# Optimization experiments

Hardware: AMD Instinct MI355X
Metric: run time of the kernel (lower is better)

## Reference

```python
import jax, jax.numpy as jnp
import numpy as np

NUM_EXPERTS = 8
EXPERTS_PER_TOK = 2

def setup_inputs() -> dict:
    key = jax.random.key(0)
    k1, k2, k3, k4, k5 = jax.random.split(key, 5)
    B, T, D, F, E = 4, 1024, 2048, 1024, NUM_EXPERTS
    return {
        "x": jax.random.normal(k1, (B, T, D), dtype=jnp.float32),
        "router_w": jax.random.normal(k2, (D, E), dtype=jnp.float32) * 0.02,
        "gate_proj": jax.random.normal(k3, (E, D, F), dtype=jnp.float32) * 0.02,
        "up_proj": jax.random.normal(k4, (E, D, F), dtype=jnp.float32) * 0.02,
        "down_proj": jax.random.normal(k5, (E, F, D), dtype=jnp.float32) * 0.02,
    }

def reference(x, router_w, gate_proj, up_proj, down_proj):
    E, K = NUM_EXPERTS, EXPERTS_PER_TOK
    # Router: softmax over experts, take top-k, renormalize.
    scores = jnp.einsum('btd,de->bte', x, router_w).astype(jnp.float32)
    routing_weights, routing_idx = jax.lax.top_k(jax.nn.softmax(scores, axis=-1), K)
    routing_weights = (routing_weights / jnp.sum(routing_weights, axis=-1, keepdims=True)).astype(x.dtype)
    # one_hot: [B,T,K,E]. Sum over K gives 0/1 dispatch mask [B,T,E]
    # (top-k indices are distinct). Weighted sum gives combine weights.
    onehot = jax.nn.one_hot(routing_idx, E, dtype=x.dtype)
    dispatch_mask = jnp.sum(onehot, axis=2)                      # [B,T,E]
    combine_weights = jnp.einsum('btke,btk->bte', onehot, routing_weights)
    # Dense masked dispatch (same math as original einsum with size-1 I axis).
    dispatched = x[:, :, None, :] * dispatch_mask[..., None]     # [B,T,E,D]
    # SwiGLU FFN for every expert, batched over E.
    gate = jnp.einsum('bted,edf->btef', dispatched, gate_proj)
    up = jnp.einsum('bted,edf->btef', dispatched, up_proj)
    act = jax.nn.silu(gate) * up                                 # [B,T,E,F]
    expert_out = jnp.einsum('btef,efd->bted', act, down_proj)    # [B,T,E,D]
    # Combine: weights already include the dispatch mask via one-hot.
    return jnp.einsum('bted,bte->btd', expert_out, combine_weights)
```

## Files before the change

kernel.cpp:

```cpp
#include <hip/hip_runtime.h>
#include <stdint.h>

#define BT 4096
#define DMODEL 2048
#define FDIM 1024
#define NEXP 8
#define NA (BT * 2)
#define MAXTILES 72

typedef __attribute__((ext_vector_type(8))) __bf16 bf16x8;
typedef __attribute__((ext_vector_type(4))) float f32x4;

__device__ __forceinline__ unsigned short f2bf(float f) {
  union { float f; unsigned int u; } v; v.f = f;
  unsigned int u = v.u;
  unsigned int r = (u + 0x7fffu + ((u >> 16) & 1u)) >> 16;
  return (unsigned short)r;
}
__device__ __forceinline__ float bf2f(unsigned short h) {
  union { unsigned int u; float f; } v; v.u = ((unsigned int)h) << 16;
  return v.f;
}

__device__ __forceinline__ void g2l16(const void* g, void* l) {
  __builtin_amdgcn_global_load_lds((const __attribute__((address_space(1))) void*)g,
                                   (__attribute__((address_space(3))) void*)l, 16, 0, 0);
}


__global__ void k_router(const float* __restrict__ x, const float* __restrict__ rw,
                         unsigned short* __restrict__ xbf,
                         int* __restrict__ tok_e, float* __restrict__ tok_w) {
  int wid = threadIdx.x >> 6;
  int lane = threadIdx.x & 63;
  int t = blockIdx.x * 4 + wid;
  float acc[8];
#pragma unroll
  for (int e = 0; e < 8; e++) acc[e] = 0.0f;
  const float* xr = x + (size_t)t * DMODEL;
  unsigned short* xbr = xbf + (size_t)t * DMODEL;
#pragma unroll
  for (int d0 = lane * 4; d0 < DMODEL; d0 += 256) {
    float4 xv = *(const float4*)(xr + d0);
    ushort4 o = make_ushort4(f2bf(xv.x), f2bf(xv.y), f2bf(xv.z), f2bf(xv.w));
    *(ushort4*)(xbr + d0) = o;
    const float* xs = &xv.x;
#pragma unroll
    for (int j = 0; j < 4; j++) {
      const float4* r4 = (const float4*)(rw + (size_t)(d0 + j) * NEXP);
      float4 ra = r4[0], rb = r4[1];
      float xj = xs[j];
      acc[0] += xj * ra.x; acc[1] += xj * ra.y; acc[2] += xj * ra.z; acc[3] += xj * ra.w;
      acc[4] += xj * rb.x; acc[5] += xj * rb.y; acc[6] += xj * rb.z; acc[7] += xj * rb.w;
    }
  }
#pragma unroll
  for (int e = 0; e < 8; e++) {
    float v = acc[e];
#pragma unroll
    for (int off = 32; off > 0; off >>= 1) v += __shfl_xor(v, off);
    acc[e] = v;
  }
  if (lane == 0) {
    int e0 = 0; float s0 = acc[0];
#pragma unroll
    for (int e = 1; e < 8; e++) if (acc[e] > s0) { s0 = acc[e]; e0 = e; }
    int e1 = (e0 == 0) ? 1 : 0; float s1 = acc[e1];
#pragma unroll
    for (int e = 0; e < 8; e++) if (e != e0 && acc[e] > s1) { s1 = acc[e]; e1 = e; }
    float w0 = 1.0f / (1.0f + __expf(s1 - s0));
    tok_e[t * 2] = e0; tok_e[t * 2 + 1] = e1;
    tok_w[t * 2] = w0; tok_w[t * 2 + 1] = 1.0f - w0;
  }
}

__global__ void k_scanbuild(const int* __restrict__ tok_e, int* __restrict__ offsets,
                            int* __restrict__ tile_e, int* __restrict__ tile_y,
                            int* __restrict__ ntiles, int* __restrict__ cursors) {
  __shared__ int hist[NEXP];
  int tid = threadIdx.x;
  if (tid < NEXP) hist[tid] = 0;
  __syncthreads();
  for (int i = tid; i < NA; i += 256) atomicAdd(&hist[tok_e[i]], 1);
  __syncthreads();
  if (tid == 0) {
    int s = 0;
    for (int e = 0; e < NEXP; e++) { offsets[e] = s; s += hist[e]; }
    offsets[NEXP] = s;
    int idx = 0;
    for (int e = 0; e < NEXP; e++) {
      int nt = (hist[e] + 127) >> 7;
      for (int y = 0; y < nt; y++) { tile_e[idx] = e; tile_y[idx] = y; idx++; }
    }
    *ntiles = idx;
    for (int i = idx; i < MAXTILES; i++) { tile_e[i] = 0; tile_y[i] = 0; }
  }
  if (tid < NEXP) cursors[tid] = 0;
}

__global__ void k_scatter(const int* __restrict__ tok_e, const float* __restrict__ tok_w,
                          const int* __restrict__ offsets, int* __restrict__ cursors,
                          int* __restrict__ assign_token, float* __restrict__ assign_w,
                          int* __restrict__ tok2pos) {
  int i = blockIdx.x * 256 + threadIdx.x;
  if (i >= NA) return;
  int e = tok_e[i];
  int pos = offsets[e] + atomicAdd(&cursors[e], 1);
  assign_token[pos] = i >> 1;
  assign_w[pos] = tok_w[i];
  tok2pos[i] = pos;
}

__global__ void k_transpose_all(const float* __restrict__ gw, const float* __restrict__ uw,
                                const float* __restrict__ dw,
                                unsigned short* __restrict__ wtgu,
                                unsigned short* __restrict__ wtd) {
  __shared__ float tile[64][65];
  int z = blockIdx.y;
  const float* src; unsigned short* dst; int N, K, Kd;
  if (z < 8)       { src = gw + (size_t)z * DMODEL * FDIM;        dst = wtgu + (size_t)z * 2 * FDIM * DMODEL;        N = FDIM;   K = DMODEL; Kd = DMODEL; }
  else if (z < 16) { src = uw + (size_t)(z - 8) * DMODEL * FDIM;  dst = wtgu + (size_t)(z - 8) * 2 * FDIM * DMODEL;  N = FDIM;   K = DMODEL; Kd = DMODEL; }
  else             { src = dw + (size_t)(z - 16) * FDIM * DMODEL; dst = wtd + (size_t)(z - 16) * FDIM * DMODEL;      N = DMODEL; K = FDIM;   Kd = FDIM; }
  int ntx = N >> 6;
  int bx = blockIdx.x;
  int n0 = (bx % ntx) * 64, k0 = (bx / ntx) * 64;
  int rr = threadIdx.x >> 4, cc = threadIdx.x & 15;
#pragma unroll
  for (int i = 0; i < 4; i++) {
    int k = rr + i * 16;
    float4 v = *(const float4*)(src + (size_t)(k0 + k) * N + n0 + cc * 4);
    tile[k][cc * 4 + 0] = v.x; tile[k][cc * 4 + 1] = v.y;
    tile[k][cc * 4 + 2] = v.z; tile[k][cc * 4 + 3] = v.w;
  }
  __syncthreads();
#pragma unroll
  for (int i = 0; i < 4; i++) {
    int n = rr + i * 16;
    int gr = n0 + n;
    int orow;
    if (z < 8)       orow = ((gr & ~31) << 1) + (gr & 31);
    else if (z < 16) orow = ((gr & ~31) << 1) + 32 + (gr & 31);
    else             orow = gr;
    ushort4 o = make_ushort4(f2bf(tile[cc * 4 + 0][n]), f2bf(tile[cc * 4 + 1][n]),
                             f2bf(tile[cc * 4 + 2][n]), f2bf(tile[cc * 4 + 3][n]));
    *(ushort4*)(dst + (size_t)orow * Kd + k0 + cc * 4) = o;
  }
}


__global__ __launch_bounds__(256, 4) void k_gemm1(
    const unsigned short* __restrict__ xbf,
    const unsigned short* __restrict__ wtgu,
    const int* __restrict__ offsets,
    const int* __restrict__ tile_e, const int* __restrict__ tile_y,
    const int* __restrict__ ntiles,
    const int* __restrict__ assign_token,
    unsigned short* __restrict__ act) {
  const int ti = blockIdx.y;
  if (ti >= *ntiles) return;
  const int e = tile_e[ti];
  const int row_beg = offsets[e], row_end = offsets[e + 1];
  const int m_base = row_beg + tile_y[ti] * 128;
  const int n_base = blockIdx.x * 128;

  __shared__ unsigned short As[128][64];
  __shared__ unsigned short Bs[128][64];

  const int tid = threadIdx.x;
  const int lane = tid & 63, wid = tid >> 6;
  const int wr = wid >> 1, wc = wid & 1;
  const int srow = wid * 8 + (lane >> 3);
  const int scol_d = (lane & 7) * 8;
  const int scol_s = ((lane & 7) ^ (lane >> 3)) * 8;
  const int sw = (lane & 7) * 8;

  const unsigned short* wb = wtgu + (size_t)e * 2 * FDIM * DMODEL + (size_t)n_base * DMODEL;

  size_t arow[4];
#pragma unroll
  for (int i = 0; i < 4; i++) {
    int slot = m_base + i * 32 + srow;
    if (slot >= row_end) slot = row_end - 1;
    arow[i] = (size_t)assign_token[slot] * DMODEL;
  }

  f32x4 acc[4][4];
#pragma unroll
  for (int m = 0; m < 4; m++)
#pragma unroll
    for (int n = 0; n < 4; n++) acc[m][n] = f32x4{0.f, 0.f, 0.f, 0.f};

  for (int k0 = 0; k0 < DMODEL; k0 += 64) {
    __syncthreads();
#pragma unroll
    for (int i = 0; i < 4; i++)
      g2l16(xbf + arow[i] + k0 + scol_s, &As[i * 32 + srow][scol_d]);
#pragma unroll
    for (int i = 0; i < 4; i++)
      g2l16(wb + (size_t)(i * 32 + srow) * DMODEL + k0 + scol_s, &Bs[i * 32 + srow][scol_d]);
    __syncthreads();

#pragma unroll
    for (int kk = 0; kk < 2; kk++) {
      const int ko = kk * 32 + (lane >> 4) * 8;
      bf16x8 a[4], b[4];
#pragma unroll
      for (int m = 0; m < 4; m++)
        a[m] = *(const bf16x8*)&As[wr * 64 + m * 16 + (lane & 15)][ko ^ sw];
#pragma unroll
      for (int n = 0; n < 4; n++)
        b[n] = *(const bf16x8*)&Bs[wc * 64 + n * 16 + (lane & 15)][ko ^ sw];
#pragma unroll
      for (int m = 0; m < 4; m++)
#pragma unroll
        for (int n = 0; n < 4; n++)
          acc[m][n] = __builtin_amdgcn_mfma_f32_16x16x32_bf16(a[m], b[n], acc[m][n], 0, 0, 0);
    }
  }

  const int cr = (lane >> 4) * 4;
  const int ccc = lane & 15;
#pragma unroll
  for (int m = 0; m < 4; m++) {
#pragma unroll
    for (int j = 0; j < 4; j++) {
      int slot = m_base + wr * 64 + m * 16 + cr + j;
      if (slot < row_end) {
        unsigned short* dst = act + (size_t)slot * FDIM + (n_base >> 1) + wc * 32 + ccc;
#pragma unroll
        for (int n = 0; n < 2; n++) {
          float g = acc[m][n][j], u = acc[m][n + 2][j];
          float h = (g / (1.0f + __expf(-g))) * u;
          dst[n * 16] = f2bf(h);
        }
      }
    }
  }
}


__global__ __launch_bounds__(256, 4) void k_gemm2(
    const unsigned short* __restrict__ act,
    const unsigned short* __restrict__ wtd,
    const int* __restrict__ offsets,
    const int* __restrict__ tile_e, const int* __restrict__ tile_y,
    const int* __restrict__ ntiles,
    const float* __restrict__ assign_w,
    unsigned short* __restrict__ out_pa) {
  const int ti = blockIdx.y;
  if (ti >= *ntiles) return;
  const int e = tile_e[ti];
  const int row_beg = offsets[e], row_end = offsets[e + 1];
  const int m_base = row_beg + tile_y[ti] * 128;
  const int n_base = blockIdx.x * 128;

  __shared__ unsigned short As[128][64];
  __shared__ unsigned short Bs[128][64];

  const int tid = threadIdx.x;
  const int lane = tid & 63, wid = tid >> 6;
  const int wr = wid >> 1, wc = wid & 1;
  const int srow = wid * 8 + (lane >> 3);
  const int scol_d = (lane & 7) * 8;
  const int scol_s = ((lane & 7) ^ (lane >> 3)) * 8;
  const int sw = (lane & 7) * 8;

  const unsigned short* wd_e = wtd + (size_t)e * DMODEL * FDIM + (size_t)n_base * FDIM;

  size_t arow[4];
#pragma unroll
  for (int i = 0; i < 4; i++) {
    int slot = m_base + i * 32 + srow;
    if (slot >= row_end) slot = row_end - 1;
    arow[i] = (size_t)slot * FDIM;
  }

  f32x4 acc[4][4];
#pragma unroll
  for (int m = 0; m < 4; m++)
#pragma unroll
    for (int n = 0; n < 4; n++) acc[m][n] = f32x4{0.f, 0.f, 0.f, 0.f};

  for (int k0 = 0; k0 < FDIM; k0 += 64) {
    __syncthreads();
#pragma unroll
    for (int i = 0; i < 4; i++)
      g2l16(act + arow[i] + k0 + scol_s, &As[i * 32 + srow][scol_d]);
#pragma unroll
    for (int i = 0; i < 4; i++)
      g2l16(wd_e + (size_t)(i * 32 + srow) * FDIM + k0 + scol_s, &Bs[i * 32 + srow][scol_d]);
    __syncthreads();

#pragma unroll
    for (int kk = 0; kk < 2; kk++) {
      const int ko = kk * 32 + (lane >> 4) * 8;
      bf16x8 a[4], b[4];
#pragma unroll
      for (int m = 0; m < 4; m++)
        a[m] = *(const bf16x8*)&As[wr * 64 + m * 16 + (lane & 15)][ko ^ sw];
#pragma unroll
      for (int n = 0; n < 4; n++)
        b[n] = *(const bf16x8*)&Bs[wc * 64 + n * 16 + (lane & 15)][ko ^ sw];
#pragma unroll
      for (int m = 0; m < 4; m++)
#pragma unroll
        for (int n = 0; n < 4; n++)
          acc[m][n] = __builtin_amdgcn_mfma_f32_16x16x32_bf16(a[m], b[n], acc[m][n], 0, 0, 0);
    }
  }

  const int cr = (lane >> 4) * 4;
  const int ccc = lane & 15;
#pragma unroll
  for (int m = 0; m < 4; m++) {
#pragma unroll
    for (int j = 0; j < 4; j++) {
      int slot = m_base + wr * 64 + m * 16 + cr + j;
      if (slot < row_end) {
        float w = assign_w[slot];
        unsigned short* dst = out_pa + (size_t)slot * DMODEL + n_base + wc * 64 + ccc;
#pragma unroll
        for (int n = 0; n < 4; n++)
          dst[n * 16] = f2bf(acc[m][n][j] * w);
      }
    }
  }
}

__global__ void k_combine(const unsigned short* __restrict__ out_pa,
                          const int* __restrict__ tok2pos,
                          float* __restrict__ out) {
  int t = blockIdx.x;
  int p0 = tok2pos[t * 2], p1 = tok2pos[t * 2 + 1];
  int c = threadIdx.x;
  const ushort4* a = (const ushort4*)(out_pa + (size_t)p0 * DMODEL + c * 8);
  const ushort4* b = (const ushort4*)(out_pa + (size_t)p1 * DMODEL + c * 8);
  ushort4 a0 = a[0], a1 = a[1], b0 = b[0], b1 = b[1];
  float* o = out + (size_t)t * DMODEL + c * 8;
  o[0] = bf2f(a0.x) + bf2f(b0.x);
  o[1] = bf2f(a0.y) + bf2f(b0.y);
  o[2] = bf2f(a0.z) + bf2f(b0.z);
  o[3] = bf2f(a0.w) + bf2f(b0.w);
  o[4] = bf2f(a1.x) + bf2f(b1.x);
  o[5] = bf2f(a1.y) + bf2f(b1.y);
  o[6] = bf2f(a1.z) + bf2f(b1.z);
  o[7] = bf2f(a1.w) + bf2f(b1.w);
}


extern "C" void kernel_launch(void* const* d_in, const int* in_sizes, int n_in,
                              void* d_out, int out_size, void* d_ws, size_t ws_size,
                              hipStream_t stream) {
  const float* x  = (const float*)d_in[0];
  const float* rw = (const float*)d_in[1];
  const float* gw = (const float*)d_in[2];
  const float* uw = (const float*)d_in[3];
  const float* dw = (const float*)d_in[4];
  float* out = (float*)d_out;

  char* ws = (char*)d_ws;
  size_t off = 0;
  auto alloc = [&](size_t bytes) {
    size_t o = off;
    off += (bytes + 255) & ~(size_t)255;
    return o;
  };
  unsigned short* xbf    = (unsigned short*)(ws + alloc((size_t)BT * DMODEL * 2));
  unsigned short* wtgu   = (unsigned short*)(ws + alloc((size_t)NEXP * 2 * FDIM * DMODEL * 2));
  unsigned short* wtd    = (unsigned short*)(ws + alloc((size_t)NEXP * DMODEL * FDIM * 2));
  unsigned short* act    = (unsigned short*)(ws + alloc((size_t)NA * FDIM * 2));
  unsigned short* out_pa = (unsigned short*)(ws + alloc((size_t)NA * DMODEL * 2));
  int*   offsets = (int*)(ws + alloc((NEXP + 1) * 4));
  int*   cursors = (int*)(ws + alloc(NEXP * 4));
  int*   tok_e   = (int*)(ws + alloc(NA * 4));
  float* tok_w   = (float*)(ws + alloc(NA * 4));
  int*   assign_token = (int*)(ws + alloc(NA * 4));
  float* assign_w     = (float*)(ws + alloc(NA * 4));
  int*   tok2pos      = (int*)(ws + alloc(NA * 4));
  int*   tile_e       = (int*)(ws + alloc(MAXTILES * 4));
  int*   tile_y       = (int*)(ws + alloc(MAXTILES * 4));
  int*   ntiles       = (int*)(ws + alloc(4));
  if (off > ws_size) return;

  k_router<<<BT / 4, 256, 0, stream>>>(x, rw, xbf, tok_e, tok_w);
  k_scanbuild<<<1, 256, 0, stream>>>(tok_e, offsets, tile_e, tile_y, ntiles, cursors);
  k_scatter<<<NA / 256, 256, 0, stream>>>(tok_e, tok_w, offsets, cursors,
                                          assign_token, assign_w, tok2pos);
  k_transpose_all<<<dim3(512, 24), 256, 0, stream>>>(gw, uw, dw, wtgu, wtd);
  k_gemm1<<<dim3(DMODEL * 2 / 128 / 2, MAXTILES), 256, 0, stream>>>(xbf, wtgu, offsets,
                                                                    tile_e, tile_y, ntiles,
                                                                    assign_token, act);
  k_gemm2<<<dim3(DMODEL / 128, MAXTILES), 256, 0, stream>>>(act, wtd, offsets,
                                                            tile_e, tile_y, ntiles,
                                                            assign_w, out_pa);
  k_combine<<<BT, 256, 0, stream>>>(out_pa, tok2pos, out);
}
```

Before: 301.0 us.

## Double-buffer GEMM tiles and fuse combine into down-proj via atomic adds

Both expert GEMMs now double-buffer their LDS tiles, issuing the next tile's global-to-LDS loads before computing on the current one, and raise wave priority around the MFMA block. The separate combine kernel and its bf16 per-assignment intermediate are removed: gemm2 atomically adds its weighted fp32 results straight into a zeroed output. This drops one kernel launch and a large intermediate write and read, at the cost of float atomics, a memset, and lower occupancy from the doubled shared memory.

```diff
diff --git a/kernel.cpp b/kernel.cpp
--- a/kernel.cpp
+++ b/kernel.cpp
@@ -11,15 +11,15 @@
 typedef __attribute__((ext_vector_type(8))) __bf16 bf16x8;
 typedef __attribute__((ext_vector_type(4))) float f32x4;
 
+#define FENCE() asm volatile("" ::: "memory")
+#define BARRIER() do { FENCE(); __builtin_amdgcn_s_barrier(); FENCE(); } while (0)
+#define VMCNT0()  asm volatile("s_waitcnt vmcnt(0)" ::: "memory")
+
 __device__ __forceinline__ unsigned short f2bf(float f) {
   union { float f; unsigned int u; } v; v.f = f;
   unsigned int u = v.u;
   unsigned int r = (u + 0x7fffu + ((u >> 16) & 1u)) >> 16;
   return (unsigned short)r;
-}
-__device__ __forceinline__ float bf2f(unsigned short h) {
-  union { unsigned int u; float f; } v; v.u = ((unsigned int)h) << 16;
-  return v.f;
 }
 
 __device__ __forceinline__ void g2l16(const void* g, void* l) {
@@ -100,15 +100,13 @@
 
 __global__ void k_scatter(const int* __restrict__ tok_e, const float* __restrict__ tok_w,
                           const int* __restrict__ offsets, int* __restrict__ cursors,
-                          int* __restrict__ assign_token, float* __restrict__ assign_w,
-                          int* __restrict__ tok2pos) {
+                          int* __restrict__ assign_token, float* __restrict__ assign_w) {
   int i = blockIdx.x * 256 + threadIdx.x;
   if (i >= NA) return;
   int e = tok_e[i];
   int pos = offsets[e] + atomicAdd(&cursors[e], 1);
   assign_token[pos] = i >> 1;
   assign_w[pos] = tok_w[i];
-  tok2pos[i] = pos;
 }
 
 __global__ void k_transpose_all(const float* __restrict__ gw, const float* __restrict__ uw,
@@ -117,10 +115,10 @@
                                 unsigned short* __restrict__ wtd) {
   __shared__ float tile[64][65];
   int z = blockIdx.y;
-  const float* src; unsigned short* dst; int N, K, Kd;
-  if (z < 8)       { src = gw + (size_t)z * DMODEL * FDIM;        dst = wtgu + (size_t)z * 2 * FDIM * DMODEL;        N = FDIM;   K = DMODEL; Kd = DMODEL; }
-  else if (z < 16) { src = uw + (size_t)(z - 8) * DMODEL * FDIM;  dst = wtgu + (size_t)(z - 8) * 2 * FDIM * DMODEL;  N = FDIM;   K = DMODEL; Kd = DMODEL; }
-  else             { src = dw + (size_t)(z - 16) * FDIM * DMODEL; dst = wtd + (size_t)(z - 16) * FDIM * DMODEL;      N = DMODEL; K = FDIM;   Kd = FDIM; }
+  const float* src; unsigned short* dst; int N, Kd;
+  if (z < 8)       { src = gw + (size_t)z * DMODEL * FDIM;        dst = wtgu + (size_t)z * 2 * FDIM * DMODEL;        N = FDIM;   Kd = DMODEL; }
+  else if (z < 16) { src = uw + (size_t)(z - 8) * DMODEL * FDIM;  dst = wtgu + (size_t)(z - 8) * 2 * FDIM * DMODEL;  N = FDIM;   Kd = DMODEL; }
+  else             { src = dw + (size_t)(z - 16) * FDIM * DMODEL; dst = wtd + (size_t)(z - 16) * FDIM * DMODEL;      N = DMODEL; Kd = FDIM; }
   int ntx = N >> 6;
   int bx = blockIdx.x;
   int n0 = (bx % ntx) * 64, k0 = (bx / ntx) * 64;
@@ -148,7 +146,7 @@
 }
 
 
-__global__ __launch_bounds__(256, 4) void k_gemm1(
+__global__ __launch_bounds__(256, 2) void k_gemm1(
     const unsigned short* __restrict__ xbf,
     const unsigned short* __restrict__ wtgu,
     const int* __restrict__ offsets,
@@ -163,8 +161,8 @@
   const int m_base = row_beg + tile_y[ti] * 128;
   const int n_base = blockIdx.x * 128;
 
-  __shared__ unsigned short As[128][64];
-  __shared__ unsigned short Bs[128][64];
+  __shared__ unsigned short As[2][128][64];
+  __shared__ unsigned short Bs[2][128][64];
 
   const int tid = threadIdx.x;
   const int lane = tid & 63, wid = tid >> 6;
@@ -190,32 +188,41 @@
 #pragma unroll
     for (int n = 0; n < 4; n++) acc[m][n] = f32x4{0.f, 0.f, 0.f, 0.f};
 
-  for (int k0 = 0; k0 < DMODEL; k0 += 64) {
-    __syncthreads();
+  auto stage = [&](int buf, int k0) {
 #pragma unroll
     for (int i = 0; i < 4; i++)
-      g2l16(xbf + arow[i] + k0 + scol_s, &As[i * 32 + srow][scol_d]);
+      g2l16(xbf + arow[i] + k0 + scol_s, &As[buf][i * 32 + srow][scol_d]);
 #pragma unroll
     for (int i = 0; i < 4; i++)
-      g2l16(wb + (size_t)(i * 32 + srow) * DMODEL + k0 + scol_s, &Bs[i * 32 + srow][scol_d]);
-    __syncthreads();
-
+      g2l16(wb + (size_t)(i * 32 + srow) * DMODEL + k0 + scol_s, &Bs[buf][i * 32 + srow][scol_d]);
+  };
+
+  const int NT = DMODEL / 64;
+  stage(0, 0);
+  VMCNT0(); BARRIER();
+
+  for (int t = 0; t < NT; ++t) {
+    const int cur = t & 1, nxt = cur ^ 1;
+    if (t + 1 < NT) stage(nxt, (t + 1) * 64);
 #pragma unroll
     for (int kk = 0; kk < 2; kk++) {
       const int ko = kk * 32 + (lane >> 4) * 8;
       bf16x8 a[4], b[4];
 #pragma unroll
       for (int m = 0; m < 4; m++)
-        a[m] = *(const bf16x8*)&As[wr * 64 + m * 16 + (lane & 15)][ko ^ sw];
+        a[m] = *(const bf16x8*)&As[cur][wr * 64 + m * 16 + (lane & 15)][ko ^ sw];
 #pragma unroll
       for (int n = 0; n < 4; n++)
-        b[n] = *(const bf16x8*)&Bs[wc * 64 + n * 16 + (lane & 15)][ko ^ sw];
+        b[n] = *(const bf16x8*)&Bs[cur][wc * 64 + n * 16 + (lane & 15)][ko ^ sw];
+      __builtin_amdgcn_s_setprio(1);
 #pragma unroll
       for (int m = 0; m < 4; m++)
 #pragma unroll
         for (int n = 0; n < 4; n++)
           acc[m][n] = __builtin_amdgcn_mfma_f32_16x16x32_bf16(a[m], b[n], acc[m][n], 0, 0, 0);
-    }
+      __builtin_amdgcn_s_setprio(0);
+    }
+    VMCNT0(); BARRIER();
   }
 
   const int cr = (lane >> 4) * 4;
@@ -239,14 +246,15 @@
 }
 
 
-__global__ __launch_bounds__(256, 4) void k_gemm2(
+__global__ __launch_bounds__(256, 2) void k_gemm2(
     const unsigned short* __restrict__ act,
     const unsigned short* __restrict__ wtd,
     const int* __restrict__ offsets,
     const int* __restrict__ tile_e, const int* __restrict__ tile_y,
     const int* __restrict__ ntiles,
+    const int* __restrict__ assign_token,
     const float* __restrict__ assign_w,
-    unsigned short* __restrict__ out_pa) {
+    float* __restrict__ out) {
   const int ti = blockIdx.y;
   if (ti >= *ntiles) return;
   const int e = tile_e[ti];
@@ -254,8 +262,8 @@
   const int m_base = row_beg + tile_y[ti] * 128;
   const int n_base = blockIdx.x * 128;
 
-  __shared__ unsigned short As[128][64];
-  __shared__ unsigned short Bs[128][64];
+  __shared__ unsigned short As[2][128][64];
+  __shared__ unsigned short Bs[2][128][64];
 
   const int tid = threadIdx.x;
   const int lane = tid & 63, wid = tid >> 6;
@@ -281,32 +289,41 @@
 #pragma unroll
     for (int n = 0; n < 4; n++) acc[m][n] = f32x4{0.f, 0.f, 0.f, 0.f};
 
-  for (int k0 = 0; k0 < FDIM; k0 += 64) {
-    __syncthreads();
+  auto stage = [&](int buf, int k0) {
 #pragma unroll
     for (int i = 0; i < 4; i++)
-      g2l16(act + arow[i] + k0 + scol_s, &As[i * 32 + srow][scol_d]);
+      g2l16(act + arow[i] + k0 + scol_s, &As[buf][i * 32 + srow][scol_d]);
 #pragma unroll
     for (int i = 0; i < 4; i++)
-      g2l16(wd_e + (size_t)(i * 32 + srow) * FDIM + k0 + scol_s, &Bs[i * 32 + srow][scol_d]);
-    __syncthreads();
-
+      g2l16(wd_e + (size_t)(i * 32 + srow) * FDIM + k0 + scol_s, &Bs[buf][i * 32 + srow][scol_d]);
+  };
+
+  const int NT = FDIM / 64;
+  stage(0, 0);
+  VMCNT0(); BARRIER();
+
+  for (int t = 0; t < NT; ++t) {
+    const int cur = t & 1, nxt = cur ^ 1;
+    if (t + 1 < NT) stage(nxt, (t + 1) * 64);
 #pragma unroll
     for (int kk = 0; kk < 2; kk++) {
       const int ko = kk * 32 + (lane >> 4) * 8;
       bf16x8 a[4], b[4];
 #pragma unroll
       for (int m = 0; m < 4; m++)
-        a[m] = *(const bf16x8*)&As[wr * 64 + m * 16 + (lane & 15)][ko ^ sw];
+        a[m] = *(const bf16x8*)&As[cur][wr * 64 + m * 16 + (lane & 15)][ko ^ sw];
 #pragma unroll
       for (int n = 0; n < 4; n++)
-        b[n] = *(const bf16x8*)&Bs[wc * 64 + n * 16 + (lane & 15)][ko ^ sw];
+        b[n] = *(const bf16x8*)&Bs[cur][wc * 64 + n * 16 + (lane & 15)][ko ^ sw];
+      __builtin_amdgcn_s_setprio(1);
 #pragma unroll
       for (int m = 0; m < 4; m++)
 #pragma unroll
         for (int n = 0; n < 4; n++)
           acc[m][n] = __builtin_amdgcn_mfma_f32_16x16x32_bf16(a[m], b[n], acc[m][n], 0, 0, 0);
-    }
+      __builtin_amdgcn_s_setprio(0);
+    }
+    VMCNT0(); BARRIER();
   }
 
   const int cr = (lane >> 4) * 4;
@@ -317,34 +334,15 @@
     for (int j = 0; j < 4; j++) {
       int slot = m_base + wr * 64 + m * 16 + cr + j;
       if (slot < row_end) {
+        int tok = assign_token[slot];
         float w = assign_w[slot];
-        unsigned short* dst = out_pa + (size_t)slot * DMODEL + n_base + wc * 64 + ccc;
+        float* dst = out + (size_t)tok * DMODEL + n_base + wc * 64 + ccc;
 #pragma unroll
         for (int n = 0; n < 4; n++)
-          dst[n * 16] = f2bf(acc[m][n][j] * w);
+          atomicAdd(&dst[n * 16], acc[m][n][j] * w);
       }
     }
   }
-}
-
-__global__ void k_combine(const unsigned short* __restrict__ out_pa,
-                          const int* __restrict__ tok2pos,
-                          float* __restrict__ out) {
-  int t = blockIdx.x;
-  int p0 = tok2pos[t * 2], p1 = tok2pos[t * 2 + 1];
-  int c = threadIdx.x;
-  const ushort4* a = (const ushort4*)(out_pa + (size_t)p0 * DMODEL + c * 8);
-  const ushort4* b = (const ushort4*)(out_pa + (size_t)p1 * DMODEL + c * 8);
-  ushort4 a0 = a[0], a1 = a[1], b0 = b[0], b1 = b[1];
-  float* o = out + (size_t)t * DMODEL + c * 8;
-  o[0] = bf2f(a0.x) + bf2f(b0.x);
-  o[1] = bf2f(a0.y) + bf2f(b0.y);
-  o[2] = bf2f(a0.z) + bf2f(b0.z);
-  o[3] = bf2f(a0.w) + bf2f(b0.w);
-  o[4] = bf2f(a1.x) + bf2f(b1.x);
-  o[5] = bf2f(a1.y) + bf2f(b1.y);
-  o[6] = bf2f(a1.z) + bf2f(b1.z);
-  o[7] = bf2f(a1.w) + bf2f(b1.w);
 }
 
 
@@ -369,29 +367,27 @@
   unsigned short* wtgu   = (unsigned short*)(ws + alloc((size_t)NEXP * 2 * FDIM * DMODEL * 2));
   unsigned short* wtd    = (unsigned short*)(ws + alloc((size_t)NEXP * DMODEL * FDIM * 2));
   unsigned short* act    = (unsigned short*)(ws + alloc((size_t)NA * FDIM * 2));
-  unsigned short* out_pa = (unsigned short*)(ws + alloc((size_t)NA * DMODEL * 2));
   int*   offsets = (int*)(ws + alloc((NEXP + 1) * 4));
   int*   cursors = (int*)(ws + alloc(NEXP * 4));
   int*   tok_e   = (int*)(ws + alloc(NA * 4));
   float* tok_w   = (float*)(ws + alloc(NA * 4));
   int*   assign_token = (int*)(ws + alloc(NA * 4));
   float* assign_w     = (float*)(ws + alloc(NA * 4));
-  int*   tok2pos      = (int*)(ws + alloc(NA * 4));
   int*   tile_e       = (int*)(ws + alloc(MAXTILES * 4));
   int*   tile_y       = (int*)(ws + alloc(MAXTILES * 4));
   int*   ntiles       = (int*)(ws + alloc(4));
   if (off > ws_size) return;
 
+  hipMemsetAsync(out, 0, (size_t)out_size * 4, stream);
   k_router<<<BT / 4, 256, 0, stream>>>(x, rw, xbf, tok_e, tok_w);
   k_scanbuild<<<1, 256, 0, stream>>>(tok_e, offsets, tile_e, tile_y, ntiles, cursors);
   k_scatter<<<NA / 256, 256, 0, stream>>>(tok_e, tok_w, offsets, cursors,
-                                          assign_token, assign_w, tok2pos);
+                                          assign_token, assign_w);
   k_transpose_all<<<dim3(512, 24), 256, 0, stream>>>(gw, uw, dw, wtgu, wtd);
-  k_gemm1<<<dim3(DMODEL * 2 / 128 / 2, MAXTILES), 256, 0, stream>>>(xbf, wtgu, offsets,
-                                                                    tile_e, tile_y, ntiles,
-                                                                    assign_token, act);
+  k_gemm1<<<dim3(DMODEL / 128, MAXTILES), 256, 0, stream>>>(xbf, wtgu, offsets,
+                                                            tile_e, tile_y, ntiles,
+                                                            assign_token, act);
   k_gemm2<<<dim3(DMODEL / 128, MAXTILES), 256, 0, stream>>>(act, wtd, offsets,
                                                             tile_e, tile_y, ntiles,
-                                                            assign_w, out_pa);
-  k_combine<<<BT, 256, 0, stream>>>(out_pa, tok2pos, out);
-}
+                                                            assign_token, assign_w, out);
+}
```

Measured after the change: 340.8 us. 13.2% more time.
